# Kernel tuning notes

Hardware: AMD Instinct MI355X
Metric: run time of the kernel (lower is better)

## Reference

```python
import jax, jax.numpy as jnp
import numpy as np

BLOCK_SIZE = 64
SKETCH_DIM = 64


def setup_inputs() -> dict:
    key = jax.random.key(0)
    k1, k2, k3, k4 = jax.random.split(key, 4)
    batch, heads, n, d = 4, 32, 8192, 128
    Q = jax.random.normal(k1, (batch, heads, n, d), dtype=jnp.float32)
    K = jax.random.normal(k2, (batch, heads, n, d), dtype=jnp.float32)
    # Rademacher +-1 diagonal
    rademacher = jnp.where(jax.random.uniform(k3, (d,)) < 0.5, -1.0, 1.0).astype(jnp.float32)
    # projection buffer as stored in the module: randn/sqrt(k) pre-scaled by rademacher rows
    projection = (jax.random.normal(k4, (d, SKETCH_DIM), dtype=jnp.float32)
                  / jnp.sqrt(jnp.float32(SKETCH_DIM))) * rademacher[:, None]
    return {"Q": Q, "K": K, "rademacher": rademacher, "projection": projection}


def _block_mean(x, B):
    # x: (batch, n, d) with n divisible by B -> (batch, n//B, d)
    b, n, d = x.shape
    return x.reshape(b, n // B, B, d).mean(axis=2)


def reference(Q, K, rademacher, projection):
    # Head averaging: (batch, n, d)
    Q_avg = Q.mean(axis=1)
    K_avg = K.mean(axis=1)
    # Token-space sketch: per-block mean over BLOCK_SIZE tokens
    Q_bar = _block_mean(Q_avg, BLOCK_SIZE)  # (batch, b_q, d)
    K_bar = _block_mean(K_avg, BLOCK_SIZE)  # (batch, b_k, d)
    # Feature-space sketch (SRHT): x * D then matmul with (D-prescaled) projection
    Q_tilde = (Q_bar * rademacher) @ projection  # (batch, b_q, k)
    K_tilde = (K_bar * rademacher) @ projection  # (batch, b_k, k)
    # Block-level attention estimate
    A_hat = jnp.einsum('bqk,bsk->bqs', Q_tilde, K_tilde) / jnp.sqrt(jnp.float32(SKETCH_DIM))
    return A_hat, Q_bar, K_bar
```

## Files before the change

### kernel.cpp

```cpp
#include <hip/hip_runtime.h>
#include <hip/hip_bf16.h>

#define BATCH   4
#define HEADS   32
#define NTOK    8192
#define DDIM    128
#define BLK     64
#define NB      (NTOK/BLK)
#define SK      64
#define OUT_QB  (BATCH*NB*NB)
#define OUT_KB  (2*BATCH*NB*NB)

__global__ __launch_bounds__(1024, 8) void bar_reduce_kernel(
    const float* __restrict__ Q, const float* __restrict__ K,
    float* __restrict__ out)
{
    const int bid    = blockIdx.x;
    const int tensor = bid >> 9;
    const int rem    = bid & 511;
    const int b      = rem >> 7;
    const int nb     = rem & 127;

    const float* base = tensor ? K : Q;
    const float* src  = base + ((size_t)b * HEADS * NTOK + (size_t)nb * BLK) * DDIM;

    const int tid  = threadIdx.x;
    const int lane = tid & 31;
    const int tg   = tid >> 5;

    float4 acc = make_float4(0.f, 0.f, 0.f, 0.f);
    #pragma unroll 4
    for (int h = 0; h < HEADS; ++h) {
        const float4* p = (const float4*)(src + (size_t)h * (NTOK * DDIM));
        float4 v0 = p[(2 * tg    ) * 32 + lane];
        float4 v1 = p[(2 * tg + 1) * 32 + lane];
        acc.x += v0.x + v1.x;
        acc.y += v0.y + v1.y;
        acc.z += v0.z + v1.z;
        acc.w += v0.w + v1.w;
    }

    __shared__ float4 red[1024];
    red[tid] = acc;
    __syncthreads();

    #pragma unroll
    for (int s = 512; s >= 32; s >>= 1) {
        if (tid < s) {
            float4 a = red[tid], c = red[tid + s];
            a.x += c.x; a.y += c.y; a.z += c.z; a.w += c.w;
            red[tid] = a;
        }
        __syncthreads();
    }

    if (tid < 32) {
        float4 s = red[tid];
        const float inv = 1.0f / (HEADS * BLK);
        s.x *= inv; s.y *= inv; s.z *= inv; s.w *= inv;
        float* dst = out + (tensor ? OUT_KB : OUT_QB) + ((size_t)b * NB + nb) * DDIM;
        ((float4*)dst)[tid] = s;
    }
}

__global__ __launch_bounds__(256) void tilde_kernel(
    const float* __restrict__ out,
    const float* __restrict__ radem,
    const float* __restrict__ proj,
    float* __restrict__ ws)
{
    const int bid     = blockIdx.x;
    const int tensor  = bid >> 4;
    const int b       = (bid >> 2) & 3;
    const int quarter = bid & 3;

    const float* bar = out + (tensor ? OUT_KB : OUT_QB)
                     + (size_t)b * (NB * DDIM) + (size_t)quarter * 32 * DDIM;
    float* dst       = ws + (size_t)tensor * (BATCH * NB * SK)
                     + (size_t)b * (NB * SK) + (size_t)quarter * 32 * SK;

    const int tid = threadIdx.x;
    const int r   = tid >> 3;
    const int kg  = (tid & 7) * 8;

    float acc[8];
    #pragma unroll
    for (int j = 0; j < 8; ++j) acc[j] = 0.f;

    #pragma unroll 4
    for (int d = 0; d < DDIM; ++d) {
        const float qv = bar[r * DDIM + d] * radem[d];
        const float4* pr = (const float4*)(proj + d * SK + kg);
        float4 p0 = pr[0], p1 = pr[1];
        acc[0] += qv * p0.x; acc[1] += qv * p0.y;
        acc[2] += qv * p0.z; acc[3] += qv * p0.w;
        acc[4] += qv * p1.x; acc[5] += qv * p1.y;
        acc[6] += qv * p1.z; acc[7] += qv * p1.w;
    }

    float4* dp = (float4*)(dst + r * SK + kg);
    dp[0] = make_float4(acc[0], acc[1], acc[2], acc[3]);
    dp[1] = make_float4(acc[4], acc[5], acc[6], acc[7]);
}

__global__ __launch_bounds__(256) void ahat_kernel(
    const float* __restrict__ ws, float* __restrict__ out)
{
    const int bid = blockIdx.x;
    const int b   = bid >> 4;
    const int qg  = bid & 15;

    const float* Qt = ws + (size_t)b * (NB * SK);
    const float* Kt = ws + (size_t)(BATCH * NB * SK) + (size_t)b * (NB * SK);

    const int tid = threadIdx.x;
    const int q   = qg * 8 + (tid >> 5);
    const int s0  = tid & 31;

    float4 qr[16];
    const float4* qp = (const float4*)(Qt + q * SK);
    #pragma unroll
    for (int i = 0; i < 16; ++i) qr[i] = qp[i];

    #pragma unroll
    for (int m = 0; m < 4; ++m) {
        const int s = s0 + m * 32;
        const float4* kp = (const float4*)(Kt + s * SK);
        float a = 0.f;
        #pragma unroll
        for (int i = 0; i < 16; ++i) {
            float4 kv = kp[i];
            a += qr[i].x * kv.x + qr[i].y * kv.y + qr[i].z * kv.z + qr[i].w * kv.w;
        }
        out[(size_t)b * (NB * NB) + q * NB + s] = a * 0.125f;
    }
}

extern "C" void kernel_launch(void* const* d_in, const int* in_sizes, int n_in,
                              void* d_out, int out_size, void* d_ws, size_t ws_size,
                              hipStream_t stream) {
    const float* Q     = (const float*)d_in[0];
    const float* K     = (const float*)d_in[1];
    const float* radem = (const float*)d_in[2];
    const float* proj  = (const float*)d_in[3];
    float* out = (float*)d_out;
    float* ws  = (float*)d_ws;

    bar_reduce_kernel<<<2 * BATCH * NB, 1024, 0, stream>>>(Q, K, out);
    tilde_kernel<<<32, 256, 0, stream>>>(out, radem, proj, ws);
    ahat_kernel<<<64, 256, 0, stream>>>(ws, out);
}
```

Baseline: 207.7 us.

## Fuse SRHT projection into bar reduction kernel and use nontemporal loads

The separate tilde kernel is folded into the reduction kernel: each block now applies the Rademacher scaling and projection to its own block mean and writes the sketched row straight to the workspace. This removes one kernel launch and a dependent global round trip. The head-sum loop now uses nontemporal vector loads and two independent accumulators to reduce cache pollution and shorten the dependency chain. The cost is an extra syncthreads and a small serial projection on 64 threads at the tail of every block, but the kernel is dominated by streaming Q and K from memory.

```diff
diff --git a/kernel.cpp b/kernel.cpp
--- a/kernel.cpp
+++ b/kernel.cpp
@@ -11,9 +11,12 @@
 #define OUT_QB  (BATCH*NB*NB)
 #define OUT_KB  (2*BATCH*NB*NB)
 
+typedef float v4f __attribute__((ext_vector_type(4)));
+
 __global__ __launch_bounds__(1024, 8) void bar_reduce_kernel(
     const float* __restrict__ Q, const float* __restrict__ K,
-    float* __restrict__ out)
+    const float* __restrict__ radem, const float* __restrict__ proj,
+    float* __restrict__ out, float* __restrict__ ws)
 {
     const int bid    = blockIdx.x;
     const int tensor = bid >> 9;
@@ -28,79 +31,59 @@
     const int lane = tid & 31;
     const int tg   = tid >> 5;
 
-    float4 acc = make_float4(0.f, 0.f, 0.f, 0.f);
+    v4f acc0 = {0.f, 0.f, 0.f, 0.f};
+    v4f acc1 = {0.f, 0.f, 0.f, 0.f};
     #pragma unroll 4
     for (int h = 0; h < HEADS; ++h) {
-        const float4* p = (const float4*)(src + (size_t)h * (NTOK * DDIM));
-        float4 v0 = p[(2 * tg    ) * 32 + lane];
-        float4 v1 = p[(2 * tg + 1) * 32 + lane];
-        acc.x += v0.x + v1.x;
-        acc.y += v0.y + v1.y;
-        acc.z += v0.z + v1.z;
-        acc.w += v0.w + v1.w;
+        const v4f* p = (const v4f*)(src + (size_t)h * (NTOK * DDIM));
+        v4f v0 = __builtin_nontemporal_load(&p[(2 * tg    ) * 32 + lane]);
+        v4f v1 = __builtin_nontemporal_load(&p[(2 * tg + 1) * 32 + lane]);
+        acc0 += v0;
+        acc1 += v1;
     }
+    v4f acc = acc0 + acc1;
 
-    __shared__ float4 red[1024];
+    __shared__ v4f   red[1024];
+    __shared__ float barS[DDIM];
     red[tid] = acc;
     __syncthreads();
 
     #pragma unroll
     for (int s = 512; s >= 32; s >>= 1) {
         if (tid < s) {
-            float4 a = red[tid], c = red[tid + s];
-            a.x += c.x; a.y += c.y; a.z += c.z; a.w += c.w;
-            red[tid] = a;
+            red[tid] += red[tid + s];
         }
         __syncthreads();
     }
 
     if (tid < 32) {
-        float4 s = red[tid];
+        v4f s = red[tid];
         const float inv = 1.0f / (HEADS * BLK);
-        s.x *= inv; s.y *= inv; s.z *= inv; s.w *= inv;
+        s *= inv;
         float* dst = out + (tensor ? OUT_KB : OUT_QB) + ((size_t)b * NB + nb) * DDIM;
-        ((float4*)dst)[tid] = s;
+        ((v4f*)dst)[tid] = s;
+        v4f rd = ((const v4f*)radem)[tid];
+        v4f sr = s * rd;
+        barS[4 * tid + 0] = sr.x;
+        barS[4 * tid + 1] = sr.y;
+        barS[4 * tid + 2] = sr.z;
+        barS[4 * tid + 3] = sr.w;
     }
-}
+    __syncthreads();
 
-__global__ __launch_bounds__(256) void tilde_kernel(
-    const float* __restrict__ out,
-    const float* __restrict__ radem,
-    const float* __restrict__ proj,
-    float* __restrict__ ws)
-{
-    const int bid     = blockIdx.x;
-    const int tensor  = bid >> 4;
-    const int b       = (bid >> 2) & 3;
-    const int quarter = bid & 3;
-
-    const float* bar = out + (tensor ? OUT_KB : OUT_QB)
-                     + (size_t)b * (NB * DDIM) + (size_t)quarter * 32 * DDIM;
-    float* dst       = ws + (size_t)tensor * (BATCH * NB * SK)
-                     + (size_t)b * (NB * SK) + (size_t)quarter * 32 * SK;
-
-    const int tid = threadIdx.x;
-    const int r   = tid >> 3;
-    const int kg  = (tid & 7) * 8;
-
-    float acc[8];
-    #pragma unroll
-    for (int j = 0; j < 8; ++j) acc[j] = 0.f;
-
-    #pragma unroll 4
-    for (int d = 0; d < DDIM; ++d) {
-        const float qv = bar[r * DDIM + d] * radem[d];
-        const float4* pr = (const float4*)(proj + d * SK + kg);
-        float4 p0 = pr[0], p1 = pr[1];
-        acc[0] += qv * p0.x; acc[1] += qv * p0.y;
-        acc[2] += qv * p0.z; acc[3] += qv * p0.w;
-        acc[4] += qv * p1.x; acc[5] += qv * p1.y;
-        acc[6] += qv * p1.z; acc[7] += qv * p1.w;
+    if (tid < SK) {
+        const int k = tid;
+        float a0 = 0.f, a1 = 0.f, a2 = 0.f, a3 = 0.f;
+        #pragma unroll 8
+        for (int d = 0; d < DDIM; d += 4) {
+            a0 += barS[d + 0] * proj[(d + 0) * SK + k];
+            a1 += barS[d + 1] * proj[(d + 1) * SK + k];
+            a2 += barS[d + 2] * proj[(d + 2) * SK + k];
+            a3 += barS[d + 3] * proj[(d + 3) * SK + k];
+        }
+        ws[((size_t)tensor * BATCH + b) * (NB * SK) + (size_t)nb * SK + k]
+            = (a0 + a1) + (a2 + a3);
     }
-
-    float4* dp = (float4*)(dst + r * SK + kg);
-    dp[0] = make_float4(acc[0], acc[1], acc[2], acc[3]);
-    dp[1] = make_float4(acc[4], acc[5], acc[6], acc[7]);
 }
 
 __global__ __launch_bounds__(256) void ahat_kernel(
@@ -146,7 +129,6 @@
     float* out = (float*)d_out;
     float* ws  = (float*)d_ws;
 
-    bar_reduce_kernel<<<2 * BATCH * NB, 1024, 0, stream>>>(Q, K, out);
-    tilde_kernel<<<32, 256, 0, stream>>>(out, radem, proj, ws);
-    ahat_kernel<<<64, 256, 0, stream>>>(ws, out);
+    bar_reduce_kernel<<<2 * BATCH * NB, 1024, 0, stream>>>(Q, K, radem, proj, out, ws);
+    ahat_kernel<<<BATCH * 16, 256, 0, stream>>>(ws, out);
 }
```

Result: faster. 172.2 us (-17.1%).
